# Optimization experiments

Measured on AMD Instinct MI355X. Metric: run time of the kernel, lower is better.

The kernel has to match this reference:

```python
import jax, jax.numpy as jnp
import numpy as np

B, N, U = 16, 1024, 64  # batch, nodes, num_units
ALPHA = 0.2  # LeakyReLU negative slope
NEG = -9e15


def setup_inputs() -> dict:
    key = jax.random.key(0)
    ks = jax.random.split(key, 7)
    X = jax.random.normal(ks[0], (B, N, U), dtype=jnp.float32)
    state = jax.random.normal(ks[1], (B, N, U), dtype=jnp.float32)
    # random sparse adjacency (avg degree ~32) with self-loops
    adj = (jax.random.uniform(ks[2], (N, N)) < 32.0 / N).astype(jnp.float32)
    adj = jnp.maximum(adj, jnp.eye(N, dtype=jnp.float32))
    def xavier(k, shape):
        fan_in, fan_out = shape
        s = 1.414 * np.sqrt(6.0 / (fan_in + fan_out))
        return jax.random.uniform(k, shape, jnp.float32, -s, s)
    W1 = xavier(ks[3], (2 * U, 2 * U))   # gat_1: in 2U -> out 2U
    a1 = xavier(ks[4], (4 * U, 1))       # attention vector, 2*out
    W2 = xavier(ks[5], (2 * U, U))       # gat_2: in 2U -> out U
    a2 = xavier(ks[6], (2 * U, 1))
    return {"X": X, "state": state, "adj": adj, "W1": W1, "a1": a1, "W2": W2, "a2": a2}


def _gat_layer(x, adj, W, a):
    # x: [b,n,f_in], W: [f_in,F], a: [2F,1]
    h = jnp.einsum('bnf,fo->bno', x, W)              # [b,n,F]
    F_out = W.shape[1]
    s_src = h @ a[:F_out, 0]                         # [b,n] contribution of node i
    s_dst = h @ a[F_out:, 0]                         # [b,n] contribution of node j
    e = jax.nn.leaky_relu(s_src[:, :, None] + s_dst[:, None, :], ALPHA)  # [b,n,n]
    e = jnp.where(adj[None, :, :] > 0, e, NEG)
    att = jax.nn.softmax(e, axis=2)                  # masked softmax over neighbors j
    return jnp.einsum('bij,bjf->bif', att, h)        # [b,n,F]


def reference(X, state, adj, W1, a1, W2, a2):
    X1 = jnp.concatenate([X, state], axis=2)         # [b,n,2U]
    gv = jax.nn.sigmoid(_gat_layer(X1, adj, W1, a1)) # [b,n,2U]
    r, z = jnp.split(gv, 2, axis=2)                  # each [b,n,U]
    X2 = jnp.concatenate([X, r * state], axis=2)
    h_t1 = jnp.tanh(_gat_layer(X2, adj, W2, a2))     # [b,n,U]
    new_h = z * state + (1.0 - z) * h_t1
    return new_h
```

## Files before the change

kernel.cpp:

```cpp
#include <hip/hip_runtime.h>
#include <hip/hip_fp16.h>

#define BB 16
#define NN 1024
#define LALPHA 0.2f
#define MAXD 192

__global__ void build_csr(const float* __restrict__ adj, int* __restrict__ deg,
                          int* __restrict__ cols) {
    __shared__ int cnt;
    int i = blockIdx.x;
    if (threadIdx.x == 0) cnt = 0;
    __syncthreads();
    for (int j = threadIdx.x; j < NN; j += blockDim.x) {
        if (adj[(size_t)i * NN + j] > 0.0f) {
            int p = atomicAdd(&cnt, 1);
            if (p < MAXD) cols[(size_t)i * MAXD + p] = j;
        }
    }
    __syncthreads();
    if (threadIdx.x == 0) deg[i] = cnt < MAXD ? cnt : MAXD;
}

template <int FOUT, int RB>
__global__ void gemm_score(const float* __restrict__ A0, const float* __restrict__ A1,
                           const float* __restrict__ W, const float* __restrict__ avec,
                           __half* __restrict__ h, float* __restrict__ s_src,
                           float* __restrict__ s_dst) {
    constexpr int TFN = FOUT / 4;
    constexpr int NT = (RB / 4) * TFN;
    __shared__ float xs[RB][132];
    int t = threadIdx.x;
    int tf = t % TFN, tr = t / TFN;
    int f0 = tf * 4, r0 = tr * 4;
    int base = blockIdx.x * RB;

    for (int idx = t; idx < RB * 32; idx += NT) {
        int r = idx >> 5, c = (idx & 31) * 4;
        float4 v = (c < 64) ? *(const float4*)(A0 + (size_t)(base + r) * 64 + c)
                            : *(const float4*)(A1 + (size_t)(base + r) * 64 + (c - 64));
        xs[r][c] = v.x; xs[r][c + 1] = v.y; xs[r][c + 2] = v.z; xs[r][c + 3] = v.w;
    }
    __syncthreads();

    float acc[4][4] = {};
    for (int k = 0; k < 128; k += 4) {
        float4 xv[4], wv[4];
#pragma unroll
        for (int i = 0; i < 4; i++) xv[i] = *(const float4*)&xs[r0 + i][k];
#pragma unroll
        for (int i = 0; i < 4; i++) wv[i] = *(const float4*)(W + (size_t)(k + i) * FOUT + f0);
#pragma unroll
        for (int i = 0; i < 4; i++) {
            float xr[4] = {xv[i].x, xv[i].y, xv[i].z, xv[i].w};
#pragma unroll
            for (int kk = 0; kk < 4; kk++) {
                acc[i][0] += xr[kk] * wv[kk].x;
                acc[i][1] += xr[kk] * wv[kk].y;
                acc[i][2] += xr[kk] * wv[kk].z;
                acc[i][3] += xr[kk] * wv[kk].w;
            }
        }
    }

    float a_s[4], a_d[4];
#pragma unroll
    for (int i = 0; i < 4; i++) {
        a_s[i] = avec[f0 + i];
        a_d[i] = avec[FOUT + f0 + i];
    }
#pragma unroll
    for (int i = 0; i < 4; i++) {
        int m = base + r0 + i;
        union { __half2 hh[2]; float2 ff; } u;
        u.hh[0] = __floats2half2_rn(acc[i][0], acc[i][1]);
        u.hh[1] = __floats2half2_rn(acc[i][2], acc[i][3]);
        *(float2*)(h + (size_t)m * FOUT + f0) = u.ff;
        float ps = acc[i][0] * a_s[0] + acc[i][1] * a_s[1] + acc[i][2] * a_s[2] + acc[i][3] * a_s[3];
        float pd = acc[i][0] * a_d[0] + acc[i][1] * a_d[1] + acc[i][2] * a_d[2] + acc[i][3] * a_d[3];
#pragma unroll
        for (int o = TFN / 2; o >= 1; o >>= 1) {
            ps += __shfl_xor(ps, o);
            pd += __shfl_xor(pd, o);
        }
        if (tf == 0) {
            s_src[m] = ps;
            s_dst[m] = pd;
        }
    }
}

__global__ __launch_bounds__(64) void attn1_fused(
    const int* __restrict__ deg, const int* __restrict__ cols,
    const __half* __restrict__ h1, const float* __restrict__ s_src,
    const float* __restrict__ s_dst, const float* __restrict__ state,
    const float* __restrict__ X, const float* __restrict__ W2,
    const float* __restrict__ a2, float* __restrict__ zbuf,
    __half* __restrict__ h2, float* __restrict__ ssrc2, float* __restrict__ sdst2) {
    int bi = blockIdx.x;
    int i = bi & (NN - 1);
    int b = bi >> 10;
    int lane = threadIdx.x;
    int d = deg[i];
    float ssrc = s_src[bi];
    __shared__ float w[MAXD];
    __shared__ int cl[MAXD];
    __shared__ __align__(16) float x2[128];
    for (int j = lane; j < d; j += 64) cl[j] = cols[(size_t)i * MAXD + j];
    __syncthreads();
    float mx = -1e30f;
    for (int j = lane; j < d; j += 64) {
        float e = ssrc + s_dst[b * NN + cl[j]];
        e = e > 0.f ? e : LALPHA * e;
        w[j] = e;
        mx = fmaxf(mx, e);
    }
#pragma unroll
    for (int o = 32; o >= 1; o >>= 1) mx = fmaxf(mx, __shfl_xor(mx, o));
    float sum = 0.f;
    for (int j = lane; j < d; j += 64) {
        float e = __expf(w[j] - mx);
        w[j] = e;
        sum += e;
    }
#pragma unroll
    for (int o = 32; o >= 1; o >>= 1) sum += __shfl_xor(sum, o);
    __syncthreads();
    float inv = 1.f / sum;

    int q = lane >> 4, fl = lane & 15;
    const __half* hb = h1 + (size_t)b * NN * 128;
    float a8[8] = {};
#pragma unroll 2
    for (int j = 0; j < d; j += 4) {
        int jj = j + q;
        float wt = (jj < d) ? w[jj] : 0.f;
        int row = cl[(jj < d) ? jj : j];
        union { float4 f; __half2 h[4]; } u;
        u.f = *(const float4*)(hb + (size_t)row * 128 + fl * 8);
#pragma unroll
        for (int k = 0; k < 4; k++) {
            a8[2 * k]     += wt * __low2float(u.h[k]);
            a8[2 * k + 1] += wt * __high2float(u.h[k]);
        }
    }
#pragma unroll
    for (int k = 0; k < 8; k++) {
        a8[k] += __shfl_xor(a8[k], 32);
        a8[k] += __shfl_xor(a8[k], 16);
    }

    size_t mo = (size_t)bi * 64;
    if (lane < 8) {
        int c = lane * 8;
        float4 s0 = *(const float4*)(state + mo + c);
        float4 s1 = *(const float4*)(state + mo + c + 4);
        float rs[8];
#pragma unroll
        for (int k = 0; k < 8; k++) rs[k] = 1.f / (1.f + __expf(-a8[k] * inv));
        *(float4*)&x2[64 + c]     = make_float4(rs[0]*s0.x, rs[1]*s0.y, rs[2]*s0.z, rs[3]*s0.w);
        *(float4*)&x2[64 + c + 4] = make_float4(rs[4]*s1.x, rs[5]*s1.y, rs[6]*s1.z, rs[7]*s1.w);
    } else if (lane < 16) {
        int c = (lane - 8) * 8;
        float zz[8];
#pragma unroll
        for (int k = 0; k < 8; k++) zz[k] = 1.f / (1.f + __expf(-a8[k] * inv));
        *(float4*)(zbuf + mo + c)     = make_float4(zz[0], zz[1], zz[2], zz[3]);
        *(float4*)(zbuf + mo + c + 4) = make_float4(zz[4], zz[5], zz[6], zz[7]);
    } else if (lane < 32) {
        *(float4*)&x2[(lane - 16) * 4] = *(const float4*)(X + mo + (lane - 16) * 4);
    }
    __syncthreads();

    float hacc = 0.f;
#pragma unroll 8
    for (int k = 0; k < 128; k += 4) {
        float4 xv = *(const float4*)&x2[k];
        hacc += xv.x * W2[(size_t)(k + 0) * 64 + lane];
        hacc += xv.y * W2[(size_t)(k + 1) * 64 + lane];
        hacc += xv.z * W2[(size_t)(k + 2) * 64 + lane];
        hacc += xv.w * W2[(size_t)(k + 3) * 64 + lane];
    }
    h2[mo + lane] = __float2half_rn(hacc);
    float ps = hacc * a2[lane];
    float pd = hacc * a2[64 + lane];
#pragma unroll
    for (int o = 32; o >= 1; o >>= 1) {
        ps += __shfl_xor(ps, o);
        pd += __shfl_xor(pd, o);
    }
    if (lane == 0) {
        ssrc2[bi] = ps;
        sdst2[bi] = pd;
    }
}

__global__ __launch_bounds__(64) void attn2_kernel(
    const int* __restrict__ deg, const int* __restrict__ cols,
    const __half* __restrict__ h2, const float* __restrict__ s_src,
    const float* __restrict__ s_dst, const float* __restrict__ state,
    const float* __restrict__ zbuf, float* __restrict__ out) {
    int bi = blockIdx.x;
    int i = bi & (NN - 1);
    int b = bi >> 10;
    int lane = threadIdx.x;
    int d = deg[i];
    float ssrc = s_src[bi];
    __shared__ float w[MAXD];
    __shared__ int cl[MAXD];
    for (int j = lane; j < d; j += 64) cl[j] = cols[(size_t)i * MAXD + j];
    __syncthreads();
    float mx = -1e30f;
    for (int j = lane; j < d; j += 64) {
        float e = ssrc + s_dst[b * NN + cl[j]];
        e = e > 0.f ? e : LALPHA * e;
        w[j] = e;
        mx = fmaxf(mx, e);
    }
#pragma unroll
    for (int o = 32; o >= 1; o >>= 1) mx = fmaxf(mx, __shfl_xor(mx, o));
    float sum = 0.f;
    for (int j = lane; j < d; j += 64) {
        float e = __expf(w[j] - mx);
        w[j] = e;
        sum += e;
    }
#pragma unroll
    for (int o = 32; o >= 1; o >>= 1) sum += __shfl_xor(sum, o);
    __syncthreads();
    float inv = 1.f / sum;

    int q = lane >> 3, fl = lane & 7;
    const __half* hb = h2 + (size_t)b * NN * 64;
    float a8[8] = {};
#pragma unroll 2
    for (int j = 0; j < d; j += 8) {
        int jj = j + q;
        float wt = (jj < d) ? w[jj] : 0.f;
        int row = cl[(jj < d) ? jj : j];
        union { float4 f; __half2 h[4]; } u;
        u.f = *(const float4*)(hb + (size_t)row * 64 + fl * 8);
#pragma unroll
        for (int k = 0; k < 4; k++) {
            a8[2 * k]     += wt * __low2float(u.h[k]);
            a8[2 * k + 1] += wt * __high2float(u.h[k]);
        }
    }
#pragma unroll
    for (int k = 0; k < 8; k++) {
        a8[k] += __shfl_xor(a8[k], 32);
        a8[k] += __shfl_xor(a8[k], 16);
        a8[k] += __shfl_xor(a8[k], 8);
    }

    if (lane < 8) {
        size_t mo = (size_t)bi * 64;
        int c = lane * 8;
        float4 z0 = *(const float4*)(zbuf + mo + c);
        float4 z1 = *(const float4*)(zbuf + mo + c + 4);
        float4 s0 = *(const float4*)(state + mo + c);
        float4 s1 = *(const float4*)(state + mo + c + 4);
        float4 o0, o1;
        o0.x = z0.x * s0.x + (1.f - z0.x) * tanhf(a8[0] * inv);
        o0.y = z0.y * s0.y + (1.f - z0.y) * tanhf(a8[1] * inv);
        o0.z = z0.z * s0.z + (1.f - z0.z) * tanhf(a8[2] * inv);
        o0.w = z0.w * s0.w + (1.f - z0.w) * tanhf(a8[3] * inv);
        o1.x = z1.x * s1.x + (1.f - z1.x) * tanhf(a8[4] * inv);
        o1.y = z1.y * s1.y + (1.f - z1.y) * tanhf(a8[5] * inv);
        o1.z = z1.z * s1.z + (1.f - z1.z) * tanhf(a8[6] * inv);
        o1.w = z1.w * s1.w + (1.f - z1.w) * tanhf(a8[7] * inv);
        *(float4*)(out + mo + c)     = o0;
        *(float4*)(out + mo + c + 4) = o1;
    }
}

extern "C" void kernel_launch(void* const* d_in, const int* in_sizes, int n_in,
                              void* d_out, int out_size, void* d_ws, size_t ws_size,
                              hipStream_t stream) {
    const float* X     = (const float*)d_in[0];
    const float* state = (const float*)d_in[1];
    const float* adj   = (const float*)d_in[2];
    const float* W1    = (const float*)d_in[3];
    const float* a1    = (const float*)d_in[4];
    const float* W2    = (const float*)d_in[5];
    const float* a2    = (const float*)d_in[6];
    float* out = (float*)d_out;

    char* ws = (char*)d_ws;
    size_t off = 0;
    auto alloc = [&](size_t bytes) -> void* {
        void* p = ws + off;
        off = (off + bytes + 255) & ~(size_t)255;
        return p;
    };
    int*    deg   = (int*)alloc(NN * sizeof(int));
    int*    cols  = (int*)alloc((size_t)NN * MAXD * sizeof(int));
    __half* h1    = (__half*)alloc((size_t)BB * NN * 128 * sizeof(__half));
    float*  ssrc1 = (float*)alloc((size_t)BB * NN * sizeof(float));
    float*  sdst1 = (float*)alloc((size_t)BB * NN * sizeof(float));
    float*  zbuf  = (float*)alloc((size_t)BB * NN * 64 * sizeof(float));
    __half* h2    = (__half*)alloc((size_t)BB * NN * 64 * sizeof(__half));
    float*  ssrc2 = (float*)alloc((size_t)BB * NN * sizeof(float));
    float*  sdst2 = (float*)alloc((size_t)BB * NN * sizeof(float));

    const int M = BB * NN;

    build_csr<<<NN, 256, 0, stream>>>(adj, deg, cols);
    gemm_score<128, 32><<<M / 32, 256, 0, stream>>>(X, state, W1, a1, h1, ssrc1, sdst1);
    attn1_fused<<<M, 64, 0, stream>>>(deg, cols, h1, ssrc1, sdst1, state, X, W2, a2,
                                      zbuf, h2, ssrc2, sdst2);
    attn2_kernel<<<M, 64, 0, stream>>>(deg, cols, h2, ssrc2, sdst2, state, zbuf, out);
}
```

Measured before the change: 137.7 us.

## Restructure GAT pipeline: merge CSR build with GEMM1, batch attention per node, split GEMM2

Merges CSR construction and the first GEMM into one launch using disjoint block ranges. The attention kernels now use one 256-thread block per node, with each wave covering four batches, so the column list is loaded once and shared across all batches. The per-row GEMV for W2 moves out of attention1 into a separate tiled GEMM kernel that reads a half-precision r*state intermediate. This adds an extra launch and an extra intermediate buffer, and quantises r*state to half, in exchange for better reuse and a GEMM with real tiling.

```diff
diff --git a/kernel.cpp b/kernel.cpp
--- a/kernel.cpp
+++ b/kernel.cpp
@@ -6,39 +6,38 @@
 #define LALPHA 0.2f
 #define MAXD 192
 
-__global__ void build_csr(const float* __restrict__ adj, int* __restrict__ deg,
-                          int* __restrict__ cols) {
+__global__ __launch_bounds__(256) void csr_gemm1(
+    const float* __restrict__ adj, const float* __restrict__ X,
+    const float* __restrict__ state, const float* __restrict__ W1,
+    const float* __restrict__ a1, int* __restrict__ deg, int* __restrict__ cols,
+    __half* __restrict__ h1, float* __restrict__ ssrc1, float* __restrict__ sdst1) {
+    __shared__ __align__(16) float xs[32][132];
     __shared__ int cnt;
-    int i = blockIdx.x;
-    if (threadIdx.x == 0) cnt = 0;
-    __syncthreads();
-    for (int j = threadIdx.x; j < NN; j += blockDim.x) {
-        if (adj[(size_t)i * NN + j] > 0.0f) {
-            int p = atomicAdd(&cnt, 1);
-            if (p < MAXD) cols[(size_t)i * MAXD + p] = j;
-        }
-    }
-    __syncthreads();
-    if (threadIdx.x == 0) deg[i] = cnt < MAXD ? cnt : MAXD;
-}
-
-template <int FOUT, int RB>
-__global__ void gemm_score(const float* __restrict__ A0, const float* __restrict__ A1,
-                           const float* __restrict__ W, const float* __restrict__ avec,
-                           __half* __restrict__ h, float* __restrict__ s_src,
-                           float* __restrict__ s_dst) {
-    constexpr int TFN = FOUT / 4;
-    constexpr int NT = (RB / 4) * TFN;
-    __shared__ float xs[RB][132];
     int t = threadIdx.x;
-    int tf = t % TFN, tr = t / TFN;
+
+    if (blockIdx.x >= 512) {
+        int i = blockIdx.x - 512;
+        if (t == 0) cnt = 0;
+        __syncthreads();
+        for (int j = t; j < NN; j += 256) {
+            if (adj[(size_t)i * NN + j] > 0.0f) {
+                int p = atomicAdd(&cnt, 1);
+                if (p < MAXD) cols[(size_t)i * MAXD + p] = j;
+            }
+        }
+        __syncthreads();
+        if (t == 0) deg[i] = cnt < MAXD ? cnt : MAXD;
+        return;
+    }
+
+    int tf = t & 31, tr = t >> 5;
     int f0 = tf * 4, r0 = tr * 4;
-    int base = blockIdx.x * RB;
-
-    for (int idx = t; idx < RB * 32; idx += NT) {
+    int base = blockIdx.x * 32;
+
+    for (int idx = t; idx < 32 * 32; idx += 256) {
         int r = idx >> 5, c = (idx & 31) * 4;
-        float4 v = (c < 64) ? *(const float4*)(A0 + (size_t)(base + r) * 64 + c)
-                            : *(const float4*)(A1 + (size_t)(base + r) * 64 + (c - 64));
+        float4 v = (c < 64) ? *(const float4*)(X + (size_t)(base + r) * 64 + c)
+                            : *(const float4*)(state + (size_t)(base + r) * 64 + (c - 64));
         xs[r][c] = v.x; xs[r][c + 1] = v.y; xs[r][c + 2] = v.z; xs[r][c + 3] = v.w;
     }
     __syncthreads();
@@ -49,7 +48,7 @@
 #pragma unroll
         for (int i = 0; i < 4; i++) xv[i] = *(const float4*)&xs[r0 + i][k];
 #pragma unroll
-        for (int i = 0; i < 4; i++) wv[i] = *(const float4*)(W + (size_t)(k + i) * FOUT + f0);
+        for (int i = 0; i < 4; i++) wv[i] = *(const float4*)(W1 + (size_t)(k + i) * 128 + f0);
 #pragma unroll
         for (int i = 0; i < 4; i++) {
             float xr[4] = {xv[i].x, xv[i].y, xv[i].z, xv[i].w};
@@ -66,8 +65,8 @@
     float a_s[4], a_d[4];
 #pragma unroll
     for (int i = 0; i < 4; i++) {
-        a_s[i] = avec[f0 + i];
-        a_d[i] = avec[FOUT + f0 + i];
+        a_s[i] = a1[f0 + i];
+        a_d[i] = a1[128 + f0 + i];
     }
 #pragma unroll
     for (int i = 0; i < 4; i++) {
@@ -75,202 +74,259 @@
         union { __half2 hh[2]; float2 ff; } u;
         u.hh[0] = __floats2half2_rn(acc[i][0], acc[i][1]);
         u.hh[1] = __floats2half2_rn(acc[i][2], acc[i][3]);
-        *(float2*)(h + (size_t)m * FOUT + f0) = u.ff;
-        float ps = acc[i][0] * a_s[0] + acc[i][1] * a_s[1] + acc[i][2] * a_s[2] + acc[i][3] * a_s[3];
-        float pd = acc[i][0] * a_d[0] + acc[i][1] * a_d[1] + acc[i][2] * a_d[2] + acc[i][3] * a_d[3];
-#pragma unroll
-        for (int o = TFN / 2; o >= 1; o >>= 1) {
+        *(float2*)(h1 + (size_t)m * 128 + f0) = u.ff;
+        float ps = acc[i][0]*a_s[0] + acc[i][1]*a_s[1] + acc[i][2]*a_s[2] + acc[i][3]*a_s[3];
+        float pd = acc[i][0]*a_d[0] + acc[i][1]*a_d[1] + acc[i][2]*a_d[2] + acc[i][3]*a_d[3];
+#pragma unroll
+        for (int o = 16; o >= 1; o >>= 1) {
             ps += __shfl_xor(ps, o);
             pd += __shfl_xor(pd, o);
         }
         if (tf == 0) {
-            s_src[m] = ps;
-            s_dst[m] = pd;
-        }
-    }
-}
-
-__global__ __launch_bounds__(64) void attn1_fused(
+            ssrc1[m] = ps;
+            sdst1[m] = pd;
+        }
+    }
+}
+
+__global__ __launch_bounds__(256) void attn1_allb(
     const int* __restrict__ deg, const int* __restrict__ cols,
-    const __half* __restrict__ h1, const float* __restrict__ s_src,
-    const float* __restrict__ s_dst, const float* __restrict__ state,
-    const float* __restrict__ X, const float* __restrict__ W2,
-    const float* __restrict__ a2, float* __restrict__ zbuf,
+    const __half* __restrict__ h1, const float* __restrict__ ssrc1,
+    const float* __restrict__ sdst1, const float* __restrict__ state,
+    float* __restrict__ zbuf, __half* __restrict__ x2u) {
+    const int i = blockIdx.x;
+    const int t = threadIdx.x, wid = t >> 6, lane = t & 63;
+    __shared__ int cl[MAXD];
+    __shared__ float wbuf[4][MAXD];
+    const int d = deg[i];
+    for (int j = t; j < d; j += 256) cl[j] = cols[(size_t)i * MAXD + j];
+    __syncthreads();
+    float* w = wbuf[wid];
+    const int q4 = lane >> 4, fl = lane & 15;
+
+#pragma unroll 1
+    for (int qq = 0; qq < 4; qq++) {
+        const int b = wid * 4 + qq;
+        const size_t mrow = (size_t)b * NN + i;
+        const float ssrc = ssrc1[mrow];
+        float mx = -1e30f;
+        for (int j = lane; j < d; j += 64) {
+            float e = ssrc + sdst1[(size_t)b * NN + cl[j]];
+            e = e > 0.f ? e : LALPHA * e;
+            w[j] = e;
+            mx = fmaxf(mx, e);
+        }
+#pragma unroll
+        for (int o = 32; o >= 1; o >>= 1) mx = fmaxf(mx, __shfl_xor(mx, o));
+        float sum = 0.f;
+        for (int j = lane; j < d; j += 64) {
+            float e = __expf(w[j] - mx);
+            w[j] = e;
+            sum += e;
+        }
+#pragma unroll
+        for (int o = 32; o >= 1; o >>= 1) sum += __shfl_xor(sum, o);
+        const float inv = 1.f / sum;
+
+        const __half* hb = h1 + (size_t)b * NN * 128;
+        float a8[8] = {};
+#pragma unroll 2
+        for (int j = 0; j < d; j += 4) {
+            int jj = j + q4;
+            float wt = (jj < d) ? w[jj] : 0.f;
+            int row = cl[(jj < d) ? jj : j];
+            union { float4 f; __half2 h[4]; } u;
+            u.f = *(const float4*)(hb + (size_t)row * 128 + fl * 8);
+#pragma unroll
+            for (int k = 0; k < 4; k++) {
+                a8[2 * k]     += wt * __low2float(u.h[k]);
+                a8[2 * k + 1] += wt * __high2float(u.h[k]);
+            }
+        }
+#pragma unroll
+        for (int k = 0; k < 8; k++) {
+            a8[k] += __shfl_xor(a8[k], 32);
+            a8[k] += __shfl_xor(a8[k], 16);
+        }
+
+        size_t mo = mrow * 64;
+        if (lane < 8) {
+            int c = lane * 8;
+            float4 s0 = *(const float4*)(state + mo + c);
+            float4 s1 = *(const float4*)(state + mo + c + 4);
+            float rs[8];
+#pragma unroll
+            for (int k = 0; k < 8; k++) rs[k] = 1.f / (1.f + __expf(-a8[k] * inv));
+            union { __half2 hh[4]; float4 ff; } u;
+            u.hh[0] = __floats2half2_rn(rs[0] * s0.x, rs[1] * s0.y);
+            u.hh[1] = __floats2half2_rn(rs[2] * s0.z, rs[3] * s0.w);
+            u.hh[2] = __floats2half2_rn(rs[4] * s1.x, rs[5] * s1.y);
+            u.hh[3] = __floats2half2_rn(rs[6] * s1.z, rs[7] * s1.w);
+            *(float4*)(x2u + mo + c) = u.ff;
+        } else if (lane < 16) {
+            int c = (lane - 8) * 8;
+            float zz[8];
+#pragma unroll
+            for (int k = 0; k < 8; k++) zz[k] = 1.f / (1.f + __expf(-a8[k] * inv));
+            *(float4*)(zbuf + mo + c)     = make_float4(zz[0], zz[1], zz[2], zz[3]);
+            *(float4*)(zbuf + mo + c + 4) = make_float4(zz[4], zz[5], zz[6], zz[7]);
+        }
+    }
+}
+
+__global__ __launch_bounds__(256) void gemm2_score(
+    const float* __restrict__ X, const __half* __restrict__ x2u,
+    const float* __restrict__ W2, const float* __restrict__ a2,
     __half* __restrict__ h2, float* __restrict__ ssrc2, float* __restrict__ sdst2) {
-    int bi = blockIdx.x;
-    int i = bi & (NN - 1);
-    int b = bi >> 10;
-    int lane = threadIdx.x;
-    int d = deg[i];
-    float ssrc = s_src[bi];
-    __shared__ float w[MAXD];
+    __shared__ __align__(16) float xs[64][132];
+    int t = threadIdx.x;
+    int tf = t & 15, tr = t >> 4;
+    int f0 = tf * 4, r0 = tr * 4;
+    int base = blockIdx.x * 64;
+
+    for (int idx = t; idx < 64 * 32; idx += 256) {
+        int r = idx >> 5, c = (idx & 31) * 4;
+        if (c < 64) {
+            float4 v = *(const float4*)(X + (size_t)(base + r) * 64 + c);
+            xs[r][c] = v.x; xs[r][c + 1] = v.y; xs[r][c + 2] = v.z; xs[r][c + 3] = v.w;
+        } else {
+            union { float2 f; __half2 h[2]; } u;
+            u.f = *(const float2*)(x2u + (size_t)(base + r) * 64 + (c - 64));
+            xs[r][c]     = __low2float(u.h[0]);
+            xs[r][c + 1] = __high2float(u.h[0]);
+            xs[r][c + 2] = __low2float(u.h[1]);
+            xs[r][c + 3] = __high2float(u.h[1]);
+        }
+    }
+    __syncthreads();
+
+    float acc[4][4] = {};
+    for (int k = 0; k < 128; k += 4) {
+        float4 xv[4], wv[4];
+#pragma unroll
+        for (int i = 0; i < 4; i++) xv[i] = *(const float4*)&xs[r0 + i][k];
+#pragma unroll
+        for (int i = 0; i < 4; i++) wv[i] = *(const float4*)(W2 + (size_t)(k + i) * 64 + f0);
+#pragma unroll
+        for (int i = 0; i < 4; i++) {
+            float xr[4] = {xv[i].x, xv[i].y, xv[i].z, xv[i].w};
+#pragma unroll
+            for (int kk = 0; kk < 4; kk++) {
+                acc[i][0] += xr[kk] * wv[kk].x;
+                acc[i][1] += xr[kk] * wv[kk].y;
+                acc[i][2] += xr[kk] * wv[kk].z;
+                acc[i][3] += xr[kk] * wv[kk].w;
+            }
+        }
+    }
+
+    float a_s[4], a_d[4];
+#pragma unroll
+    for (int i = 0; i < 4; i++) {
+        a_s[i] = a2[f0 + i];
+        a_d[i] = a2[64 + f0 + i];
+    }
+#pragma unroll
+    for (int i = 0; i < 4; i++) {
+        int m = base + r0 + i;
+        union { __half2 hh[2]; float2 ff; } u;
+        u.hh[0] = __floats2half2_rn(acc[i][0], acc[i][1]);
+        u.hh[1] = __floats2half2_rn(acc[i][2], acc[i][3]);
+        *(float2*)(h2 + (size_t)m * 64 + f0) = u.ff;
+        float ps = acc[i][0]*a_s[0] + acc[i][1]*a_s[1] + acc[i][2]*a_s[2] + acc[i][3]*a_s[3];
+        float pd = acc[i][0]*a_d[0] + acc[i][1]*a_d[1] + acc[i][2]*a_d[2] + acc[i][3]*a_d[3];
+#pragma unroll
+        for (int o = 8; o >= 1; o >>= 1) {
+            ps += __shfl_xor(ps, o);
+            pd += __shfl_xor(pd, o);
+        }
+        if (tf == 0) {
+            ssrc2[m] = ps;
+            sdst2[m] = pd;
+        }
+    }
+}
+
+__global__ __launch_bounds__(256) void attn2_allb(
+    const int* __restrict__ deg, const int* __restrict__ cols,
+    const __half* __restrict__ h2, const float* __restrict__ ssrc2,
+    const float* __restrict__ sdst2, const float* __restrict__ state,
+    const float* __restrict__ zbuf, float* __restrict__ out) {
+    const int i = blockIdx.x;
+    const int t = threadIdx.x, wid = t >> 6, lane = t & 63;
     __shared__ int cl[MAXD];
-    __shared__ __align__(16) float x2[128];
-    for (int j = lane; j < d; j += 64) cl[j] = cols[(size_t)i * MAXD + j];
+    __shared__ float wbuf[4][MAXD];
+    const int d = deg[i];
+    for (int j = t; j < d; j += 256) cl[j] = cols[(size_t)i * MAXD + j];
     __syncthreads();
-    float mx = -1e30f;
-    for (int j = lane; j < d; j += 64) {
-        float e = ssrc + s_dst[b * NN + cl[j]];
-        e = e > 0.f ? e : LALPHA * e;
-        w[j] = e;
-        mx = fmaxf(mx, e);
-    }
-#pragma unroll
-    for (int o = 32; o >= 1; o >>= 1) mx = fmaxf(mx, __shfl_xor(mx, o));
-    float sum = 0.f;
-    for (int j = lane; j < d; j += 64) {
-        float e = __expf(w[j] - mx);
-        w[j] = e;
-        sum += e;
-    }
-#pragma unroll
-    for (int o = 32; o >= 1; o >>= 1) sum += __shfl_xor(sum, o);
-    __syncthreads();
-    float inv = 1.f / sum;
-
-    int q = lane >> 4, fl = lane & 15;
-    const __half* hb = h1 + (size_t)b * NN * 128;
-    float a8[8] = {};
+    float* w = wbuf[wid];
+    const int q8 = lane >> 3, fl = lane & 7;
+
+#pragma unroll 1
+    for (int qq = 0; qq < 4; qq++) {
+        const int b = wid * 4 + qq;
+        const size_t mrow = (size_t)b * NN + i;
+        const float ssrc = ssrc2[mrow];
+        float mx = -1e30f;
+        for (int j = lane; j < d; j += 64) {
+            float e = ssrc + sdst2[(size_t)b * NN + cl[j]];
+            e = e > 0.f ? e : LALPHA * e;
+            w[j] = e;
+            mx = fmaxf(mx, e);
+        }
+#pragma unroll
+        for (int o = 32; o >= 1; o >>= 1) mx = fmaxf(mx, __shfl_xor(mx, o));
+        float sum = 0.f;
+        for (int j = lane; j < d; j += 64) {
+            float e = __expf(w[j] - mx);
+            w[j] = e;
+            sum += e;
+        }
+#pragma unroll
+        for (int o = 32; o >= 1; o >>= 1) sum += __shfl_xor(sum, o);
+        const float inv = 1.f / sum;
+
+        const __half* hb = h2 + (size_t)b * NN * 64;
+        float a8[8] = {};
 #pragma unroll 2
-    for (int j = 0; j < d; j += 4) {
-        int jj = j + q;
-        float wt = (jj < d) ? w[jj] : 0.f;
-        int row = cl[(jj < d) ? jj : j];
-        union { float4 f; __half2 h[4]; } u;
-        u.f = *(const float4*)(hb + (size_t)row * 128 + fl * 8);
-#pragma unroll
-        for (int k = 0; k < 4; k++) {
-            a8[2 * k]     += wt * __low2float(u.h[k]);
-            a8[2 * k + 1] += wt * __high2float(u.h[k]);
-        }
-    }
-#pragma unroll
-    for (int k = 0; k < 8; k++) {
-        a8[k] += __shfl_xor(a8[k], 32);
-        a8[k] += __shfl_xor(a8[k], 16);
-    }
-
-    size_t mo = (size_t)bi * 64;
-    if (lane < 8) {
-        int c = lane * 8;
-        float4 s0 = *(const float4*)(state + mo + c);
-        float4 s1 = *(const float4*)(state + mo + c + 4);
-        float rs[8];
-#pragma unroll
-        for (int k = 0; k < 8; k++) rs[k] = 1.f / (1.f + __expf(-a8[k] * inv));
-        *(float4*)&x2[64 + c]     = make_float4(rs[0]*s0.x, rs[1]*s0.y, rs[2]*s0.z, rs[3]*s0.w);
-        *(float4*)&x2[64 + c + 4] = make_float4(rs[4]*s1.x, rs[5]*s1.y, rs[6]*s1.z, rs[7]*s1.w);
-    } else if (lane < 16) {
-        int c = (lane - 8) * 8;
-        float zz[8];
-#pragma unroll
-        for (int k = 0; k < 8; k++) zz[k] = 1.f / (1.f + __expf(-a8[k] * inv));
-        *(float4*)(zbuf + mo + c)     = make_float4(zz[0], zz[1], zz[2], zz[3]);
-        *(float4*)(zbuf + mo + c + 4) = make_float4(zz[4], zz[5], zz[6], zz[7]);
-    } else if (lane < 32) {
-        *(float4*)&x2[(lane - 16) * 4] = *(const float4*)(X + mo + (lane - 16) * 4);
-    }
-    __syncthreads();
-
-    float hacc = 0.f;
-#pragma unroll 8
-    for (int k = 0; k < 128; k += 4) {
-        float4 xv = *(const float4*)&x2[k];
-        hacc += xv.x * W2[(size_t)(k + 0) * 64 + lane];
-        hacc += xv.y * W2[(size_t)(k + 1) * 64 + lane];
-        hacc += xv.z * W2[(size_t)(k + 2) * 64 + lane];
-        hacc += xv.w * W2[(size_t)(k + 3) * 64 + lane];
-    }
-    h2[mo + lane] = __float2half_rn(hacc);
-    float ps = hacc * a2[lane];
-    float pd = hacc * a2[64 + lane];
-#pragma unroll
-    for (int o = 32; o >= 1; o >>= 1) {
-        ps += __shfl_xor(ps, o);
-        pd += __shfl_xor(pd, o);
-    }
-    if (lane == 0) {
-        ssrc2[bi] = ps;
-        sdst2[bi] = pd;
-    }
-}
-
-__global__ __launch_bounds__(64) void attn2_kernel(
-    const int* __restrict__ deg, const int* __restrict__ cols,
-    const __half* __restrict__ h2, const float* __restrict__ s_src,
-    const float* __restrict__ s_dst, const float* __restrict__ state,
-    const float* __restrict__ zbuf, float* __restrict__ out) {
-    int bi = blockIdx.x;
-    int i = bi & (NN - 1);
-    int b = bi >> 10;
-    int lane = threadIdx.x;
-    int d = deg[i];
-    float ssrc = s_src[bi];
-    __shared__ float w[MAXD];
-    __shared__ int cl[MAXD];
-    for (int j = lane; j < d; j += 64) cl[j] = cols[(size_t)i * MAXD + j];
-    __syncthreads();
-    float mx = -1e30f;
-    for (int j = lane; j < d; j += 64) {
-        float e = ssrc + s_dst[b * NN + cl[j]];
-        e = e > 0.f ? e : LALPHA * e;
-        w[j] = e;
-        mx = fmaxf(mx, e);
-    }
-#pragma unroll
-    for (int o = 32; o >= 1; o >>= 1) mx = fmaxf(mx, __shfl_xor(mx, o));
-    float sum = 0.f;
-    for (int j = lane; j < d; j += 64) {
-        float e = __expf(w[j] - mx);
-        w[j] = e;
-        sum += e;
-    }
-#pragma unroll
-    for (int o = 32; o >= 1; o >>= 1) sum += __shfl_xor(sum, o);
-    __syncthreads();
-    float inv = 1.f / sum;
-
-    int q = lane >> 3, fl = lane & 7;
-    const __half* hb = h2 + (size_t)b * NN * 64;
-    float a8[8] = {};
-#pragma unroll 2
-    for (int j = 0; j < d; j += 8) {
-        int jj = j + q;
-        float wt = (jj < d) ? w[jj] : 0.f;
-        int row = cl[(jj < d) ? jj : j];
-        union { float4 f; __half2 h[4]; } u;
-        u.f = *(const float4*)(hb + (size_t)row * 64 + fl * 8);
-#pragma unroll
-        for (int k = 0; k < 4; k++) {
-            a8[2 * k]     += wt * __low2float(u.h[k]);
-            a8[2 * k + 1] += wt * __high2float(u.h[k]);
-        }
-    }
-#pragma unroll
-    for (int k = 0; k < 8; k++) {
-        a8[k] += __shfl_xor(a8[k], 32);
-        a8[k] += __shfl_xor(a8[k], 16);
-        a8[k] += __shfl_xor(a8[k], 8);
-    }
-
-    if (lane < 8) {
-        size_t mo = (size_t)bi * 64;
-        int c = lane * 8;
-        float4 z0 = *(const float4*)(zbuf + mo + c);
-        float4 z1 = *(const float4*)(zbuf + mo + c + 4);
-        float4 s0 = *(const float4*)(state + mo + c);
-        float4 s1 = *(const float4*)(state + mo + c + 4);
-        float4 o0, o1;
-        o0.x = z0.x * s0.x + (1.f - z0.x) * tanhf(a8[0] * inv);
-        o0.y = z0.y * s0.y + (1.f - z0.y) * tanhf(a8[1] * inv);
-        o0.z = z0.z * s0.z + (1.f - z0.z) * tanhf(a8[2] * inv);
-        o0.w = z0.w * s0.w + (1.f - z0.w) * tanhf(a8[3] * inv);
-        o1.x = z1.x * s1.x + (1.f - z1.x) * tanhf(a8[4] * inv);
-        o1.y = z1.y * s1.y + (1.f - z1.y) * tanhf(a8[5] * inv);
-        o1.z = z1.z * s1.z + (1.f - z1.z) * tanhf(a8[6] * inv);
-        o1.w = z1.w * s1.w + (1.f - z1.w) * tanhf(a8[7] * inv);
-        *(float4*)(out + mo + c)     = o0;
-        *(float4*)(out + mo + c + 4) = o1;
+        for (int j = 0; j < d; j += 8) {
+            int jj = j + q8;
+            float wt = (jj < d) ? w[jj] : 0.f;
+            int row = cl[(jj < d) ? jj : j];
+            union { float4 f; __half2 h[4]; } u;
+            u.f = *(const float4*)(hb + (size_t)row * 64 + fl * 8);
+#pragma unroll
+            for (int k = 0; k < 4; k++) {
+                a8[2 * k]     += wt * __low2float(u.h[k]);
+                a8[2 * k + 1] += wt * __high2float(u.h[k]);
+            }
+        }
+#pragma unroll
+        for (int k = 0; k < 8; k++) {
+            a8[k] += __shfl_xor(a8[k], 32);
+            a8[k] += __shfl_xor(a8[k], 16);
+            a8[k] += __shfl_xor(a8[k], 8);
+        }
+
+        if (lane < 8) {
+            size_t mo = mrow * 64;
+            int c = lane * 8;
+            float4 z0 = *(const float4*)(zbuf + mo + c);
+            float4 z1 = *(const float4*)(zbuf + mo + c + 4);
+            float4 s0 = *(const float4*)(state + mo + c);
+            float4 s1 = *(const float4*)(state + mo + c + 4);
+            float4 o0, o1;
+            o0.x = z0.x * s0.x + (1.f - z0.x) * tanhf(a8[0] * inv);
+            o0.y = z0.y * s0.y + (1.f - z0.y) * tanhf(a8[1] * inv);
+            o0.z = z0.z * s0.z + (1.f - z0.z) * tanhf(a8[2] * inv);
+            o0.w = z0.w * s0.w + (1.f - z0.w) * tanhf(a8[3] * inv);
+            o1.x = z1.x * s1.x + (1.f - z1.x) * tanhf(a8[4] * inv);
+            o1.y = z1.y * s1.y + (1.f - z1.y) * tanhf(a8[5] * inv);
+            o1.z = z1.z * s1.z + (1.f - z1.z) * tanhf(a8[6] * inv);
+            o1.w = z1.w * s1.w + (1.f - z1.w) * tanhf(a8[7] * inv);
+            *(float4*)(out + mo + c)     = o0;
+            *(float4*)(out + mo + c + 4) = o1;
+        }
     }
 }
 
@@ -299,15 +355,16 @@
     float*  ssrc1 = (float*)alloc((size_t)BB * NN * sizeof(float));
     float*  sdst1 = (float*)alloc((size_t)BB * NN * sizeof(float));
     float*  zbuf  = (float*)alloc((size_t)BB * NN * 64 * sizeof(float));
+    __half* x2u   = (__half*)alloc((size_t)BB * NN * 64 * sizeof(__half));
     __half* h2    = (__half*)alloc((size_t)BB * NN * 64 * sizeof(__half));
     float*  ssrc2 = (float*)alloc((size_t)BB * NN * sizeof(float));
     float*  sdst2 = (float*)alloc((size_t)BB * NN * sizeof(float));
 
     const int M = BB * NN;
 
-    build_csr<<<NN, 256, 0, stream>>>(adj, deg, cols);
-    gemm_score<128, 32><<<M / 32, 256, 0, stream>>>(X, state, W1, a1, h1, ssrc1, sdst1);
-    attn1_fused<<<M, 64, 0, stream>>>(deg, cols, h1, ssrc1, sdst1, state, X, W2, a2,
-                                      zbuf, h2, ssrc2, sdst2);
-    attn2_kernel<<<M, 64, 0, stream>>>(deg, cols, h2, ssrc2, sdst2, state, zbuf, out);
-}
+    csr_gemm1<<<512 + NN, 256, 0, stream>>>(adj, X, state, W1, a1, deg, cols,
+                                            h1, ssrc1, sdst1);
+    attn1_allb<<<NN, 256, 0, stream>>>(deg, cols, h1, ssrc1, sdst1, state, zbuf, x2u);
+    gemm2_score<<<M / 64, 256, 0, stream>>>(X, x2u, W2, a2, h2, ssrc2, sdst2);
+    attn2_allb<<<NN, 256, 0, stream>>>(deg, cols, h2, ssrc2, sdst2, state, zbuf, out);
+}
```

Result: slower. 142.3 us (+3.4%).
